# Optimization experiments

Measured on AMD Instinct MI355X. Metric: run time of the kernel, lower is better.

## Reference

```python
import jax, jax.numpy as jnp
import numpy as np

N = 100000
E = 1600000
IN_C, HID_C, OUT_C = 128, 128, 64


def setup_inputs() -> dict:
    key = jax.random.key(0)
    k_x, k_e, k_w1, k_w2 = jax.random.split(key, 4)
    x = jax.random.normal(k_x, (N, IN_C), dtype=jnp.float32)
    edge_index = jax.random.randint(k_e, (2, E), 0, N, dtype=jnp.int32)
    # nn.Linear default init: U(-1/sqrt(fan_in), 1/sqrt(fan_in)); bias init zeros per module
    lim1 = 1.0 / np.sqrt(IN_C)
    lim2 = 1.0 / np.sqrt(HID_C)
    W1 = jax.random.uniform(k_w1, (IN_C, HID_C), minval=-lim1, maxval=lim1, dtype=jnp.float32)
    b1 = jnp.zeros((HID_C,), dtype=jnp.float32)
    W2 = jax.random.uniform(k_w2, (HID_C, OUT_C), minval=-lim2, maxval=lim2, dtype=jnp.float32)
    b2 = jnp.zeros((OUT_C,), dtype=jnp.float32)
    return {"x": x, "edge_index": edge_index, "W1": W1, "b1": b1, "W2": W2, "b2": b2}


def _out_degree_gcn_conv(x, src, dst, W, b, n_nodes):
    # linear projection (no bias in lin)
    h = x @ W  # [N, out_c]
    # out-degree of each source node
    deg = jax.ops.segment_sum(jnp.ones((src.shape[0],), dtype=h.dtype), src, num_segments=n_nodes)
    deg_inv = 1.0 / jnp.maximum(deg, 1.0)  # clamp(min=1)
    h = h * deg_inv[:, None]
    # message: x_j = h[src]; aggregate: sum at dst
    out = jax.ops.segment_sum(h[src], dst, num_segments=n_nodes)  # [N, out_c]
    return out + b


def reference(x, edge_index, W1, b1, W2, b2):
    src, dst = edge_index[0], edge_index[1]
    n = x.shape[0]
    h = _out_degree_gcn_conv(x, src, dst, W1, b1, n)
    h = jax.nn.relu(h)
    # dropout p=0.0 -> identity
    out = _out_degree_gcn_conv(h, src, dst, W2, b2, n)
    return out
```

## Files before the change

kernel.cpp:

```cpp
#include <hip/hip_runtime.h>
#include <hip/hip_bf16.h>


typedef __attribute__((ext_vector_type(8))) short short8;
typedef __attribute__((ext_vector_type(4))) float floatx4;

__device__ inline unsigned short f2bf(float f) {
    union { float f; unsigned u; } v; v.f = f;
    return (unsigned short)((v.u + 0x8000u) >> 16);
}
__device__ inline float bf2f(unsigned b) {
    union { unsigned u; float f; } v; v.u = b << 16;
    return v.f;
}
__device__ inline float bf2f_hi(unsigned b) {
    union { unsigned u; float f; } v; v.u = b & 0xFFFF0000u;
    return v.f;
}

#define NBMAX 512
#define CAP   8192

__global__ __launch_bounds__(256) void convw_kernel(
    const float* __restrict__ W1, const float* __restrict__ W2,
    unsigned short* __restrict__ Wb1, unsigned short* __restrict__ Wb2,
    int* __restrict__ cnt)
{
    int i = blockIdx.x * 256 + threadIdx.x;
    if (i < NBMAX * 32) cnt[i] = 0;
    if (i < 128 * 128) {
        int k = i >> 7, n = i & 127;
        Wb1[n * 128 + k] = f2bf(W1[k * 128 + n]);
    }
    i -= 128 * 128;
    if (i >= 0 && i < 128 * 64) {
        int k = i >> 6, n = i & 63;
        Wb2[n * 128 + k] = f2bf(W2[k * 64 + n]);
    }
}

__global__ __launch_bounds__(256) void scatter2_kernel(
    const int* __restrict__ src, const int* __restrict__ dst, int E,
    int* __restrict__ cnt_d, int* __restrict__ cnt_s,
    unsigned* __restrict__ pairs, unsigned char* __restrict__ srcs_b, int NB,
    const float* __restrict__ x, unsigned short* __restrict__ xb, int NF8)
{
    const int EB = (E + 8191) / 8192;
    if ((int)blockIdx.x >= EB) {
        int i = ((int)blockIdx.x - EB) * 256 + threadIdx.x;
        if (i < NF8) {
            float4 a0 = ((const float4*)x)[(size_t)i * 2];
            float4 a1 = ((const float4*)x)[(size_t)i * 2 + 1];
            uint4 st;
            st.x = (unsigned)f2bf(a0.x) | ((unsigned)f2bf(a0.y) << 16);
            st.y = (unsigned)f2bf(a0.z) | ((unsigned)f2bf(a0.w) << 16);
            st.z = (unsigned)f2bf(a1.x) | ((unsigned)f2bf(a1.y) << 16);
            st.w = (unsigned)f2bf(a1.z) | ((unsigned)f2bf(a1.w) << 16);
            ((uint4*)xb)[i] = st;
        }
        return;
    }
    __shared__ int hd[NBMAX], bd[NBMAX], cd_[NBMAX];
    __shared__ int hs[NBMAX], bs[NBMAX], cs_[NBMAX];
    for (int i = threadIdx.x; i < NB; i += 256) { hd[i] = 0; cd_[i] = 0; hs[i] = 0; cs_[i] = 0; }
    __syncthreads();
    const int e0 = blockIdx.x * 8192;
    const int e1 = min(e0 + 8192, E);
    for (int i = e0 + threadIdx.x; i < e1; i += 256) {
        atomicAdd(&hd[dst[i] >> 8], 1);
        atomicAdd(&hs[src[i] >> 8], 1);
    }
    __syncthreads();
    for (int i = threadIdx.x; i < NB; i += 256) {
        if (hd[i]) bd[i] = atomicAdd(&cnt_d[i * 16], hd[i]);
        if (hs[i]) bs[i] = atomicAdd(&cnt_s[i * 16], hs[i]);
    }
    __syncthreads();
    for (int i = e0 + threadIdx.x; i < e1; i += 256) {
        int sv = src[i], dv = dst[i];
        int b = dv >> 8;
        int slot = atomicAdd(&cd_[b], 1);
        pairs[(size_t)b * CAP + bd[b] + slot] = ((unsigned)(dv & 255) << 24) | (unsigned)sv;
        int b2 = sv >> 8;
        int slot2 = atomicAdd(&cs_[b2], 1);
        srcs_b[(size_t)b2 * CAP + bs[b2] + slot2] = (unsigned char)(sv & 255);
    }
}

__global__ __launch_bounds__(256) void bucket_finalize_kernel(
    const unsigned* __restrict__ pairs, const unsigned char* __restrict__ srcs_b,
    const int* __restrict__ cnt_d, const int* __restrict__ cnt_s,
    int* __restrict__ sorted_src, int2* __restrict__ se,
    float* __restrict__ deg_inv, int N)
{
    const int b = blockIdx.x;
    const int node0 = b << 8;
    const int t = threadIdx.x;
    const size_t base = (size_t)b * CAP;
    __shared__ int hist[256];
    __shared__ int cur[256];
    __shared__ int pre[256];

    const int cd = cnt_d[b * 16];
    hist[t] = 0;
    __syncthreads();
    for (int i = t; i < cd; i += 256)
        atomicAdd(&hist[pairs[base + i] >> 24], 1);
    __syncthreads();
    int v = hist[t];
    int v4 = (v + 3) & ~3;
    pre[t] = v4;
    __syncthreads();
    for (int o = 1; o < 256; o <<= 1) {
        int add = (t >= o) ? pre[t - o] : 0;
        __syncthreads();
        pre[t] += add;
        __syncthreads();
    }
    int excl = pre[t] - v4;
    cur[t] = excl;
    if (node0 + t < N) {
        se[node0 + t] = make_int2((int)base + excl, (int)base + excl + v);
        for (int i = v; i < v4; ++i) sorted_src[base + excl + i] = N;
    }
    __syncthreads();
    for (int i = t; i < cd; i += 256) {
        unsigned p = pairs[base + i];
        int pos = atomicAdd(&cur[p >> 24], 1);
        sorted_src[base + pos] = (int)(p & 0xFFFFFFu);
    }

    __syncthreads();
    hist[t] = 0;
    __syncthreads();
    const int cs = cnt_s[b * 16];
    for (int i = t; i < cs; i += 256)
        atomicAdd(&hist[srcs_b[base + i]], 1);
    __syncthreads();
    if (node0 + t < N) {
        int d = hist[t];
        deg_inv[node0 + t] = 1.0f / (float)(d < 1 ? 1 : d);
    }
}

template <int NC, int SC>
__global__ __launch_bounds__(256) void gemm_mfma_kernel(
    const unsigned short* __restrict__ Ab, const unsigned short* __restrict__ Wb,
    const float* __restrict__ scale, unsigned short* __restrict__ Cb, int M)
{
    constexpr int NT = NC / 16;
    const int t = threadIdx.x;
    if (blockIdx.x == 0 && t < NC / 2)
        ((unsigned*)Cb)[(size_t)M * (NC / 2) + t] = 0;
    const int wm = t >> 6;
    const int lane = t & 63;
    const int lm = lane & 15;
    const int lk = (lane >> 4) * 8;

    const int r0 = blockIdx.x * 64 + wm * 16;
    int row = r0 + lm;
    if (row >= M) row = M - 1;

    floatx4 acc[NT];
#pragma unroll
    for (int j = 0; j < NT; ++j) acc[j] = (floatx4){0.f, 0.f, 0.f, 0.f};

#pragma unroll
    for (int kk = 0; kk < 4; ++kk) {
        const int kb = kk * 32 + lk;
        short8 af = *(const short8*)&Ab[(size_t)row * 128 + kb];
#pragma unroll
        for (int j = 0; j < NT; ++j) {
            short8 bfr = *(const short8*)&Wb[(size_t)(j * 16 + lm) * 128 + kb];
            acc[j] = __builtin_amdgcn_mfma_f32_16x16x32_bf16(af, bfr, acc[j], 0, 0, 0);
        }
    }

    const int rbase = r0 + (lane >> 4) * 4;
#pragma unroll
    for (int reg = 0; reg < 4; ++reg) {
        int rg = rbase + reg;
        if (rg < M) {
            float di = SC ? scale[rg] : 1.0f;
#pragma unroll
            for (int j = 0; j < NT; ++j)
                Cb[(size_t)rg * NC + j * 16 + lm] = f2bf(SC ? acc[j][reg] * di : acc[j][reg]);
        }
    }
}

#define LD128(vv, ii) uint2 vv = *(const uint2*)&val[(size_t)(ii) * 64 + 2 * l]
#define ACC8_128(I0, I1) do { \
    LD128(v0, I0.x); LD128(v1, I0.y); LD128(v2, I0.z); LD128(v3, I0.w); \
    LD128(v4, I1.x); LD128(v5, I1.y); LD128(v6, I1.z); LD128(v7, I1.w); \
    a0 += ((bf2f(v0.x & 0xFFFF) + bf2f(v1.x & 0xFFFF)) + (bf2f(v2.x & 0xFFFF) + bf2f(v3.x & 0xFFFF))) \
        + ((bf2f(v4.x & 0xFFFF) + bf2f(v5.x & 0xFFFF)) + (bf2f(v6.x & 0xFFFF) + bf2f(v7.x & 0xFFFF))); \
    a1 += ((bf2f_hi(v0.x) + bf2f_hi(v1.x)) + (bf2f_hi(v2.x) + bf2f_hi(v3.x))) \
        + ((bf2f_hi(v4.x) + bf2f_hi(v5.x)) + (bf2f_hi(v6.x) + bf2f_hi(v7.x))); \
    a2 += ((bf2f(v0.y & 0xFFFF) + bf2f(v1.y & 0xFFFF)) + (bf2f(v2.y & 0xFFFF) + bf2f(v3.y & 0xFFFF))) \
        + ((bf2f(v4.y & 0xFFFF) + bf2f(v5.y & 0xFFFF)) + (bf2f(v6.y & 0xFFFF) + bf2f(v7.y & 0xFFFF))); \
    a3 += ((bf2f_hi(v0.y) + bf2f_hi(v1.y)) + (bf2f_hi(v2.y) + bf2f_hi(v3.y))) \
        + ((bf2f_hi(v4.y) + bf2f_hi(v5.y)) + (bf2f_hi(v6.y) + bf2f_hi(v7.y))); \
} while (0)
#define ACC4_128(I0) do { \
    LD128(v0, I0.x); LD128(v1, I0.y); LD128(v2, I0.z); LD128(v3, I0.w); \
    a0 += (bf2f(v0.x & 0xFFFF) + bf2f(v1.x & 0xFFFF)) + (bf2f(v2.x & 0xFFFF) + bf2f(v3.x & 0xFFFF)); \
    a1 += (bf2f_hi(v0.x) + bf2f_hi(v1.x)) + (bf2f_hi(v2.x) + bf2f_hi(v3.x)); \
    a2 += (bf2f(v0.y & 0xFFFF) + bf2f(v1.y & 0xFFFF)) + (bf2f(v2.y & 0xFFFF) + bf2f(v3.y & 0xFFFF)); \
    a3 += (bf2f_hi(v0.y) + bf2f_hi(v1.y)) + (bf2f_hi(v2.y) + bf2f_hi(v3.y)); \
} while (0)

__global__ __launch_bounds__(256) void aggregate128_kernel(
    const int2* __restrict__ se, const int* __restrict__ sorted_src,
    const unsigned* __restrict__ val, const float* __restrict__ bias,
    const float* __restrict__ deg_inv, unsigned* __restrict__ outb, int N)
{
    const int hw = threadIdx.x >> 5;
    const int l = threadIdx.x & 31;
    for (int g = 0; g < 4; ++g) {
        int node = blockIdx.x * 32 + g * 8 + hw;
        if (node >= N) continue;
        int2 r = se[node];
        int e = r.x;
        const int end4 = r.x + ((r.y - r.x + 3) & ~3);
        float a0 = 0.f, a1 = 0.f, a2 = 0.f, a3 = 0.f;

        if (e + 8 <= end4) {
            int4 i0 = *(const int4*)&sorted_src[e];
            int4 i1 = *(const int4*)&sorted_src[e + 4];
            for (; e + 16 <= end4; e += 8) {
                int4 n0 = *(const int4*)&sorted_src[e + 8];
                int4 n1 = *(const int4*)&sorted_src[e + 12];
                ACC8_128(i0, i1);
                i0 = n0; i1 = n1;
            }
            ACC8_128(i0, i1);
            e += 8;
        }
        if (e < end4) {
            int4 i0 = *(const int4*)&sorted_src[e];
            ACC4_128(i0);
        }

        float di = deg_inv[node];
        float4 bv = *(const float4*)&bias[4 * l];
        a0 = fmaxf(a0 + bv.x, 0.f) * di;
        a1 = fmaxf(a1 + bv.y, 0.f) * di;
        a2 = fmaxf(a2 + bv.z, 0.f) * di;
        a3 = fmaxf(a3 + bv.w, 0.f) * di;
        uint2 o;
        o.x = (unsigned)f2bf(a0) | ((unsigned)f2bf(a1) << 16);
        o.y = (unsigned)f2bf(a2) | ((unsigned)f2bf(a3) << 16);
        *(uint2*)&outb[(size_t)node * 64 + 2 * l] = o;
    }
}

#define LD64(vv, ii) unsigned vv = val[(size_t)(ii) * 32 + l]
#define ACC8_64(I0, I1) do { \
    LD64(v0, I0.x); LD64(v1, I0.y); LD64(v2, I0.z); LD64(v3, I0.w); \
    LD64(v4, I1.x); LD64(v5, I1.y); LD64(v6, I1.z); LD64(v7, I1.w); \
    ax += ((bf2f(v0 & 0xFFFF) + bf2f(v1 & 0xFFFF)) + (bf2f(v2 & 0xFFFF) + bf2f(v3 & 0xFFFF))) \
        + ((bf2f(v4 & 0xFFFF) + bf2f(v5 & 0xFFFF)) + (bf2f(v6 & 0xFFFF) + bf2f(v7 & 0xFFFF))); \
    ay += ((bf2f_hi(v0) + bf2f_hi(v1)) + (bf2f_hi(v2) + bf2f_hi(v3))) \
        + ((bf2f_hi(v4) + bf2f_hi(v5)) + (bf2f_hi(v6) + bf2f_hi(v7))); \
} while (0)
#define ACC4_64(I0) do { \
    LD64(v0, I0.x); LD64(v1, I0.y); LD64(v2, I0.z); LD64(v3, I0.w); \
    ax += (bf2f(v0 & 0xFFFF) + bf2f(v1 & 0xFFFF)) + (bf2f(v2 & 0xFFFF) + bf2f(v3 & 0xFFFF)); \
    ay += (bf2f_hi(v0) + bf2f_hi(v1)) + (bf2f_hi(v2) + bf2f_hi(v3)); \
} while (0)

__global__ __launch_bounds__(256) void aggregate64_kernel(
    const int2* __restrict__ se, const int* __restrict__ sorted_src,
    const unsigned* __restrict__ val, const float* __restrict__ bias,
    float* __restrict__ out, int N)
{
    const int hw = threadIdx.x >> 5;
    const int l = threadIdx.x & 31;
    for (int g = 0; g < 4; ++g) {
        int node = blockIdx.x * 32 + g * 8 + hw;
        if (node >= N) continue;
        int2 r = se[node];
        int e = r.x;
        const int end4 = r.x + ((r.y - r.x + 3) & ~3);
        float ax = 0.f, ay = 0.f;

        if (e + 8 <= end4) {
            int4 i0 = *(const int4*)&sorted_src[e];
            int4 i1 = *(const int4*)&sorted_src[e + 4];
            for (; e + 16 <= end4; e += 8) {
                int4 n0 = *(const int4*)&sorted_src[e + 8];
                int4 n1 = *(const int4*)&sorted_src[e + 12];
                ACC8_64(i0, i1);
                i0 = n0; i1 = n1;
            }
            ACC8_64(i0, i1);
            e += 8;
        }
        if (e < end4) {
            int4 i0 = *(const int4*)&sorted_src[e];
            ACC4_64(i0);
        }

        float2 o = make_float2(ax + bias[2 * l], ay + bias[2 * l + 1]);
        *(float2*)&out[(size_t)node * 64 + 2 * l] = o;
    }
}

extern "C" void kernel_launch(void* const* d_in, const int* in_sizes, int n_in,
                              void* d_out, int out_size, void* d_ws, size_t ws_size,
                              hipStream_t stream) {
    const float* x  = (const float*)d_in[0];
    const int*   ei = (const int*)d_in[1];
    const float* W1 = (const float*)d_in[2];
    const float* b1 = (const float*)d_in[3];
    const float* W2 = (const float*)d_in[4];
    const float* b2 = (const float*)d_in[5];
    float* out = (float*)d_out;

    const int N = in_sizes[0] / 128;
    const int E = in_sizes[1] / 2;
    const int* src = ei;
    const int* dst = ei + E;
    const int NB = (N + 255) >> 8;

    char* ws = (char*)d_ws;
    size_t off = 0;
    auto alloc = [&](size_t bytes) {
        void* p = ws + off;
        off = (off + bytes + 255) & ~(size_t)255;
        return p;
    };
    float* deg_inv  = (float*)alloc((size_t)N * 4);
    int2*  se       = (int2*)alloc((size_t)N * 8);
    int*   cnt_d    = (int*)alloc((size_t)NBMAX * 16 * 4 * 2);
    int*   cnt_s    = cnt_d + (size_t)NBMAX * 16;
    unsigned short* Wb1 = (unsigned short*)alloc((size_t)128 * 128 * 2);
    unsigned short* Wb2 = (unsigned short*)alloc((size_t)64 * 128 * 2);
    unsigned*      pairs  = (unsigned*)alloc((size_t)NBMAX * CAP * 4);
    unsigned char* srcs_b = (unsigned char*)alloc((size_t)NBMAX * CAP);
    int*   sorted_src = (int*)alloc((size_t)NBMAX * CAP * 4);
    unsigned short* h    = (unsigned short*)alloc((size_t)(N + 1) * 128 * 2);
    unsigned short* out1 = (unsigned short*)alloc((size_t)N * 128 * 2);
    unsigned short* xb = out1;
    unsigned short* g = ((size_t)(N + 1) * 128 <= (size_t)NBMAX * CAP * 4)
                            ? (unsigned short*)pairs
                            : (unsigned short*)alloc((size_t)(N + 1) * 64 * 2);

    convw_kernel<<<96, 256, 0, stream>>>(W1, W2, Wb1, Wb2, cnt_d);

    const int EB = (E + 8191) / 8192;
    const int NF8 = (N * 128) / 8;
    const int CB = (NF8 + 255) / 256;
    scatter2_kernel<<<EB + CB, 256, 0, stream>>>(src, dst, E, cnt_d, cnt_s,
                                                 pairs, srcs_b, NB, x, xb, NF8);
    bucket_finalize_kernel<<<NB, 256, 0, stream>>>(pairs, srcs_b, cnt_d, cnt_s,
                                                   sorted_src, se, deg_inv, N);

    const int gblocks = (N + 63) / 64;
    const int ablocks = (N + 31) / 32;
    gemm_mfma_kernel<128, 1><<<gblocks, 256, 0, stream>>>(xb, Wb1, deg_inv, h, N);
    aggregate128_kernel<<<ablocks, 256, 0, stream>>>(se, sorted_src, (const unsigned*)h, b1,
                                                     deg_inv, (unsigned*)out1, N);
    gemm_mfma_kernel<64, 0><<<gblocks, 256, 0, stream>>>(out1, Wb2, nullptr, g, N);
    aggregate64_kernel<<<ablocks, 256, 0, stream>>>(se, sorted_src, (const unsigned*)g, b2, out, N);
}
```

Baseline: 316.8 us.

## Count out-degree with global atomics, enlarge scatter blocks, one node per half-warp

Replaces the per-bucket byte scatter of source ids plus the second histogram pass with direct global atomic increments into a per-node degree array, which is zeroed in the weight-conversion kernel. This removes the srcs_b buffer and its writes and reads. The scatter kernel moves to 1024-thread blocks. Both aggregate kernels now handle one node per half-warp with 8 nodes per block instead of looping over 32 nodes, giving four times more blocks. The trade is 1.6M global atomics on a 100K-entry array, which may contend.

```diff
diff --git a/kernel.cpp b/kernel.cpp
--- a/kernel.cpp
+++ b/kernel.cpp
@@ -24,10 +24,11 @@
 __global__ __launch_bounds__(256) void convw_kernel(
     const float* __restrict__ W1, const float* __restrict__ W2,
     unsigned short* __restrict__ Wb1, unsigned short* __restrict__ Wb2,
-    int* __restrict__ cnt)
+    int* __restrict__ cnt_d, int* __restrict__ deg_cnt, int N)
 {
     int i = blockIdx.x * 256 + threadIdx.x;
-    if (i < NBMAX * 32) cnt[i] = 0;
+    if (i < NBMAX * 16) cnt_d[i] = 0;
+    if (i < N) deg_cnt[i] = 0;
     if (i < 128 * 128) {
         int k = i >> 7, n = i & 127;
         Wb1[n * 128 + k] = f2bf(W1[k * 128 + n]);
@@ -39,15 +40,15 @@
     }
 }
 
-__global__ __launch_bounds__(256) void scatter2_kernel(
+__global__ __launch_bounds__(1024) void scatter2_kernel(
     const int* __restrict__ src, const int* __restrict__ dst, int E,
-    int* __restrict__ cnt_d, int* __restrict__ cnt_s,
-    unsigned* __restrict__ pairs, unsigned char* __restrict__ srcs_b, int NB,
+    int* __restrict__ cnt_d, int* __restrict__ deg_cnt,
+    unsigned* __restrict__ pairs, int NB,
     const float* __restrict__ x, unsigned short* __restrict__ xb, int NF8)
 {
     const int EB = (E + 8191) / 8192;
     if ((int)blockIdx.x >= EB) {
-        int i = ((int)blockIdx.x - EB) * 256 + threadIdx.x;
+        int i = ((int)blockIdx.x - EB) * 1024 + threadIdx.x;
         if (i < NF8) {
             float4 a0 = ((const float4*)x)[(size_t)i * 2];
             float4 a1 = ((const float4*)x)[(size_t)i * 2 + 1];
@@ -61,35 +62,30 @@
         return;
     }
     __shared__ int hd[NBMAX], bd[NBMAX], cd_[NBMAX];
-    __shared__ int hs[NBMAX], bs[NBMAX], cs_[NBMAX];
-    for (int i = threadIdx.x; i < NB; i += 256) { hd[i] = 0; cd_[i] = 0; hs[i] = 0; cs_[i] = 0; }
+    const int t = threadIdx.x;
+    for (int i = t; i < NB; i += 1024) { hd[i] = 0; cd_[i] = 0; }
     __syncthreads();
     const int e0 = blockIdx.x * 8192;
     const int e1 = min(e0 + 8192, E);
-    for (int i = e0 + threadIdx.x; i < e1; i += 256) {
+    for (int i = e0 + t; i < e1; i += 1024) {
         atomicAdd(&hd[dst[i] >> 8], 1);
-        atomicAdd(&hs[src[i] >> 8], 1);
-    }
-    __syncthreads();
-    for (int i = threadIdx.x; i < NB; i += 256) {
+        atomicAdd(&deg_cnt[src[i]], 1);
+    }
+    __syncthreads();
+    for (int i = t; i < NB; i += 1024)
         if (hd[i]) bd[i] = atomicAdd(&cnt_d[i * 16], hd[i]);
-        if (hs[i]) bs[i] = atomicAdd(&cnt_s[i * 16], hs[i]);
-    }
-    __syncthreads();
-    for (int i = e0 + threadIdx.x; i < e1; i += 256) {
+    __syncthreads();
+    for (int i = e0 + t; i < e1; i += 1024) {
         int sv = src[i], dv = dst[i];
         int b = dv >> 8;
         int slot = atomicAdd(&cd_[b], 1);
         pairs[(size_t)b * CAP + bd[b] + slot] = ((unsigned)(dv & 255) << 24) | (unsigned)sv;
-        int b2 = sv >> 8;
-        int slot2 = atomicAdd(&cs_[b2], 1);
-        srcs_b[(size_t)b2 * CAP + bs[b2] + slot2] = (unsigned char)(sv & 255);
     }
 }
 
 __global__ __launch_bounds__(256) void bucket_finalize_kernel(
-    const unsigned* __restrict__ pairs, const unsigned char* __restrict__ srcs_b,
-    const int* __restrict__ cnt_d, const int* __restrict__ cnt_s,
+    const unsigned* __restrict__ pairs, const int* __restrict__ cnt_d,
+    const int* __restrict__ deg_cnt,
     int* __restrict__ sorted_src, int2* __restrict__ se,
     float* __restrict__ deg_inv, int N)
 {
@@ -122,24 +118,14 @@
     if (node0 + t < N) {
         se[node0 + t] = make_int2((int)base + excl, (int)base + excl + v);
         for (int i = v; i < v4; ++i) sorted_src[base + excl + i] = N;
+        int d = deg_cnt[node0 + t];
+        deg_inv[node0 + t] = 1.0f / (float)(d < 1 ? 1 : d);
     }
     __syncthreads();
     for (int i = t; i < cd; i += 256) {
         unsigned p = pairs[base + i];
         int pos = atomicAdd(&cur[p >> 24], 1);
         sorted_src[base + pos] = (int)(p & 0xFFFFFFu);
-    }
-
-    __syncthreads();
-    hist[t] = 0;
-    __syncthreads();
-    const int cs = cnt_s[b * 16];
-    for (int i = t; i < cs; i += 256)
-        atomicAdd(&hist[srcs_b[base + i]], 1);
-    __syncthreads();
-    if (node0 + t < N) {
-        int d = hist[t];
-        deg_inv[node0 + t] = 1.0f / (float)(d < 1 ? 1 : d);
     }
 }
 
@@ -215,44 +201,41 @@
     const unsigned* __restrict__ val, const float* __restrict__ bias,
     const float* __restrict__ deg_inv, unsigned* __restrict__ outb, int N)
 {
-    const int hw = threadIdx.x >> 5;
-    const int l = threadIdx.x & 31;
-    for (int g = 0; g < 4; ++g) {
-        int node = blockIdx.x * 32 + g * 8 + hw;
-        if (node >= N) continue;
-        int2 r = se[node];
-        int e = r.x;
-        const int end4 = r.x + ((r.y - r.x + 3) & ~3);
-        float a0 = 0.f, a1 = 0.f, a2 = 0.f, a3 = 0.f;
-
-        if (e + 8 <= end4) {
-            int4 i0 = *(const int4*)&sorted_src[e];
-            int4 i1 = *(const int4*)&sorted_src[e + 4];
-            for (; e + 16 <= end4; e += 8) {
-                int4 n0 = *(const int4*)&sorted_src[e + 8];
-                int4 n1 = *(const int4*)&sorted_src[e + 12];
-                ACC8_128(i0, i1);
-                i0 = n0; i1 = n1;
-            }
+    int node = blockIdx.x * 8 + (threadIdx.x >> 5);
+    if (node >= N) return;
+    int l = threadIdx.x & 31;
+    int2 r = se[node];
+    int e = r.x;
+    const int end4 = r.x + ((r.y - r.x + 3) & ~3);
+    float a0 = 0.f, a1 = 0.f, a2 = 0.f, a3 = 0.f;
+
+    if (e + 8 <= end4) {
+        int4 i0 = *(const int4*)&sorted_src[e];
+        int4 i1 = *(const int4*)&sorted_src[e + 4];
+        for (; e + 16 <= end4; e += 8) {
+            int4 n0 = *(const int4*)&sorted_src[e + 8];
+            int4 n1 = *(const int4*)&sorted_src[e + 12];
             ACC8_128(i0, i1);
-            e += 8;
-        }
-        if (e < end4) {
-            int4 i0 = *(const int4*)&sorted_src[e];
-            ACC4_128(i0);
-        }
-
-        float di = deg_inv[node];
-        float4 bv = *(const float4*)&bias[4 * l];
-        a0 = fmaxf(a0 + bv.x, 0.f) * di;
-        a1 = fmaxf(a1 + bv.y, 0.f) * di;
-        a2 = fmaxf(a2 + bv.z, 0.f) * di;
-        a3 = fmaxf(a3 + bv.w, 0.f) * di;
-        uint2 o;
-        o.x = (unsigned)f2bf(a0) | ((unsigned)f2bf(a1) << 16);
-        o.y = (unsigned)f2bf(a2) | ((unsigned)f2bf(a3) << 16);
-        *(uint2*)&outb[(size_t)node * 64 + 2 * l] = o;
-    }
+            i0 = n0; i1 = n1;
+        }
+        ACC8_128(i0, i1);
+        e += 8;
+    }
+    if (e < end4) {
+        int4 i0 = *(const int4*)&sorted_src[e];
+        ACC4_128(i0);
+    }
+
+    float di = deg_inv[node];
+    float4 bv = *(const float4*)&bias[4 * l];
+    a0 = fmaxf(a0 + bv.x, 0.f) * di;
+    a1 = fmaxf(a1 + bv.y, 0.f) * di;
+    a2 = fmaxf(a2 + bv.z, 0.f) * di;
+    a3 = fmaxf(a3 + bv.w, 0.f) * di;
+    uint2 o;
+    o.x = (unsigned)f2bf(a0) | ((unsigned)f2bf(a1) << 16);
+    o.y = (unsigned)f2bf(a2) | ((unsigned)f2bf(a3) << 16);
+    *(uint2*)&outb[(size_t)node * 64 + 2 * l] = o;
 }
 
 #define LD64(vv, ii) unsigned vv = val[(size_t)(ii) * 32 + l]
@@ -275,36 +258,33 @@
     const unsigned* __restrict__ val, const float* __restrict__ bias,
     float* __restrict__ out, int N)
 {
-    const int hw = threadIdx.x >> 5;
-    const int l = threadIdx.x & 31;
-    for (int g = 0; g < 4; ++g) {
-        int node = blockIdx.x * 32 + g * 8 + hw;
-        if (node >= N) continue;
-        int2 r = se[node];
-        int e = r.x;
-        const int end4 = r.x + ((r.y - r.x + 3) & ~3);
-        float ax = 0.f, ay = 0.f;
-
-        if (e + 8 <= end4) {
-            int4 i0 = *(const int4*)&sorted_src[e];
-            int4 i1 = *(const int4*)&sorted_src[e + 4];
-            for (; e + 16 <= end4; e += 8) {
-                int4 n0 = *(const int4*)&sorted_src[e + 8];
-                int4 n1 = *(const int4*)&sorted_src[e + 12];
-                ACC8_64(i0, i1);
-                i0 = n0; i1 = n1;
-            }
+    int node = blockIdx.x * 8 + (threadIdx.x >> 5);
+    if (node >= N) return;
+    int l = threadIdx.x & 31;
+    int2 r = se[node];
+    int e = r.x;
+    const int end4 = r.x + ((r.y - r.x + 3) & ~3);
+    float ax = 0.f, ay = 0.f;
+
+    if (e + 8 <= end4) {
+        int4 i0 = *(const int4*)&sorted_src[e];
+        int4 i1 = *(const int4*)&sorted_src[e + 4];
+        for (; e + 16 <= end4; e += 8) {
+            int4 n0 = *(const int4*)&sorted_src[e + 8];
+            int4 n1 = *(const int4*)&sorted_src[e + 12];
             ACC8_64(i0, i1);
-            e += 8;
-        }
-        if (e < end4) {
-            int4 i0 = *(const int4*)&sorted_src[e];
-            ACC4_64(i0);
-        }
-
-        float2 o = make_float2(ax + bias[2 * l], ay + bias[2 * l + 1]);
-        *(float2*)&out[(size_t)node * 64 + 2 * l] = o;
-    }
+            i0 = n0; i1 = n1;
+        }
+        ACC8_64(i0, i1);
+        e += 8;
+    }
+    if (e < end4) {
+        int4 i0 = *(const int4*)&sorted_src[e];
+        ACC4_64(i0);
+    }
+
+    float2 o = make_float2(ax + bias[2 * l], ay + bias[2 * l + 1]);
+    *(float2*)&out[(size_t)node * 64 + 2 * l] = o;
 }
 
 extern "C" void kernel_launch(void* const* d_in, const int* in_sizes, int n_in,
@@ -332,13 +312,12 @@
         return p;
     };
     float* deg_inv  = (float*)alloc((size_t)N * 4);
+    int*   deg_cnt  = (int*)alloc((size_t)N * 4);
     int2*  se       = (int2*)alloc((size_t)N * 8);
-    int*   cnt_d    = (int*)alloc((size_t)NBMAX * 16 * 4 * 2);
-    int*   cnt_s    = cnt_d + (size_t)NBMAX * 16;
+    int*   cnt_d    = (int*)alloc((size_t)NBMAX * 16 * 4);
     unsigned short* Wb1 = (unsigned short*)alloc((size_t)128 * 128 * 2);
     unsigned short* Wb2 = (unsigned short*)alloc((size_t)64 * 128 * 2);
     unsigned*      pairs  = (unsigned*)alloc((size_t)NBMAX * CAP * 4);
-    unsigned char* srcs_b = (unsigned char*)alloc((size_t)NBMAX * CAP);
     int*   sorted_src = (int*)alloc((size_t)NBMAX * CAP * 4);
     unsigned short* h    = (unsigned short*)alloc((size_t)(N + 1) * 128 * 2);
     unsigned short* out1 = (unsigned short*)alloc((size_t)N * 128 * 2);
@@ -347,18 +326,19 @@
                             ? (unsigned short*)pairs
                             : (unsigned short*)alloc((size_t)(N + 1) * 64 * 2);
 
-    convw_kernel<<<96, 256, 0, stream>>>(W1, W2, Wb1, Wb2, cnt_d);
+    const int cwblocks = (N > 128 * 128 + 128 * 64 ? N + 255 : 128 * 128 + 128 * 64 + 255) / 256;
+    convw_kernel<<<cwblocks, 256, 0, stream>>>(W1, W2, Wb1, Wb2, cnt_d, deg_cnt, N);
 
     const int EB = (E + 8191) / 8192;
     const int NF8 = (N * 128) / 8;
-    const int CB = (NF8 + 255) / 256;
-    scatter2_kernel<<<EB + CB, 256, 0, stream>>>(src, dst, E, cnt_d, cnt_s,
-                                                 pairs, srcs_b, NB, x, xb, NF8);
-    bucket_finalize_kernel<<<NB, 256, 0, stream>>>(pairs, srcs_b, cnt_d, cnt_s,
+    const int CB = (NF8 + 1023) / 1024;
+    scatter2_kernel<<<EB + CB, 1024, 0, stream>>>(src, dst, E, cnt_d, deg_cnt,
+                                                  pairs, NB, x, xb, NF8);
+    bucket_finalize_kernel<<<NB, 256, 0, stream>>>(pairs, cnt_d, deg_cnt,
                                                    sorted_src, se, deg_inv, N);
 
     const int gblocks = (N + 63) / 64;
-    const int ablocks = (N + 31) / 32;
+    const int ablocks = (N + 7) / 8;
     gemm_mfma_kernel<128, 1><<<gblocks, 256, 0, stream>>>(xb, Wb1, deg_inv, h, N);
     aggregate128_kernel<<<ablocks, 256, 0, stream>>>(se, sorted_src, (const unsigned*)h, b1,
                                                      deg_inv, (unsigned*)out1, N);
```

New measurement: 327.5 us. 3.4% more time.

## Stage bucket scatter in shared memory for coalesced writes; one node per half-warp

Applied to the files above, without the earlier changes.

The edge bucketing kernel now sorts each chunk's entries by bucket in shared memory, using a local histogram and prefix scan, before writing them out. Each global write then lands in a contiguous run per bucket instead of a random address per edge. The kernel runs with 512 threads and handles the dst and src passes one after another, adding scans, a binary search per element and extra barriers. Separately, the aggregate kernels drop the 4-iteration node loop so each 32-lane group handles a single node, which launches more blocks and improves load balance.

```diff
diff --git a/kernel.cpp b/kernel.cpp
--- a/kernel.cpp
+++ b/kernel.cpp
@@ -20,6 +20,7 @@
 
 #define NBMAX 512
 #define CAP   8192
+#define CHUNK 8192
 
 __global__ __launch_bounds__(256) void convw_kernel(
     const float* __restrict__ W1, const float* __restrict__ W2,
@@ -39,15 +40,23 @@
     }
 }
 
-__global__ __launch_bounds__(256) void scatter2_kernel(
+#define SCAN512(lb, t)                                    \
+    for (int o = 1; o < 512; o <<= 1) {                   \
+        int add_ = ((t) >= o) ? lb[(t) - o] : 0;          \
+        __syncthreads();                                  \
+        lb[t] += add_;                                    \
+        __syncthreads();                                  \
+    }
+
+__global__ __launch_bounds__(512) void scatter2_kernel(
     const int* __restrict__ src, const int* __restrict__ dst, int E,
     int* __restrict__ cnt_d, int* __restrict__ cnt_s,
     unsigned* __restrict__ pairs, unsigned char* __restrict__ srcs_b, int NB,
     const float* __restrict__ x, unsigned short* __restrict__ xb, int NF8)
 {
-    const int EB = (E + 8191) / 8192;
+    const int EB = (E + CHUNK - 1) / CHUNK;
     if ((int)blockIdx.x >= EB) {
-        int i = ((int)blockIdx.x - EB) * 256 + threadIdx.x;
+        int i = ((int)blockIdx.x - EB) * 512 + threadIdx.x;
         if (i < NF8) {
             float4 a0 = ((const float4*)x)[(size_t)i * 2];
             float4 a1 = ((const float4*)x)[(size_t)i * 2 + 1];
@@ -60,30 +69,63 @@
         }
         return;
     }
-    __shared__ int hd[NBMAX], bd[NBMAX], cd_[NBMAX];
-    __shared__ int hs[NBMAX], bs[NBMAX], cs_[NBMAX];
-    for (int i = threadIdx.x; i < NB; i += 256) { hd[i] = 0; cd_[i] = 0; hs[i] = 0; cs_[i] = 0; }
-    __syncthreads();
-    const int e0 = blockIdx.x * 8192;
-    const int e1 = min(e0 + 8192, E);
-    for (int i = e0 + threadIdx.x; i < e1; i += 256) {
+    __shared__ int hd[NBMAX], lb[512], bd[NBMAX], cd_[NBMAX];
+    __shared__ unsigned staged[CHUNK];
+    const int t = threadIdx.x;
+    const int e0 = blockIdx.x * CHUNK;
+    const int e1 = min(e0 + CHUNK, E);
+    const int cnt = e1 - e0;
+
+    for (int i = t; i < NB; i += 512) { hd[i] = 0; cd_[i] = 0; }
+    __syncthreads();
+    for (int i = e0 + t; i < e1; i += 512)
         atomicAdd(&hd[dst[i] >> 8], 1);
-        atomicAdd(&hs[src[i] >> 8], 1);
-    }
-    __syncthreads();
-    for (int i = threadIdx.x; i < NB; i += 256) {
+    __syncthreads();
+    lb[t] = (t < NB) ? hd[t] : 0;
+    __syncthreads();
+    SCAN512(lb, t)
+    for (int i = t; i < NB; i += 512)
         if (hd[i]) bd[i] = atomicAdd(&cnt_d[i * 16], hd[i]);
-        if (hs[i]) bs[i] = atomicAdd(&cnt_s[i * 16], hs[i]);
-    }
-    __syncthreads();
-    for (int i = e0 + threadIdx.x; i < e1; i += 256) {
+    __syncthreads();
+    for (int i = e0 + t; i < e1; i += 512) {
         int sv = src[i], dv = dst[i];
         int b = dv >> 8;
         int slot = atomicAdd(&cd_[b], 1);
-        pairs[(size_t)b * CAP + bd[b] + slot] = ((unsigned)(dv & 255) << 24) | (unsigned)sv;
-        int b2 = sv >> 8;
-        int slot2 = atomicAdd(&cs_[b2], 1);
-        srcs_b[(size_t)b2 * CAP + bs[b2] + slot2] = (unsigned char)(sv & 255);
+        staged[lb[b] - hd[b] + slot] = ((unsigned)(dv & 255) << 24) | (unsigned)sv;
+    }
+    __syncthreads();
+    for (int i = t; i < cnt; i += 512) {
+        int lo = 0, hi = NB - 1;
+        while (lo < hi) { int mid = (lo + hi) >> 1; if (lb[mid] > i) hi = mid; else lo = mid + 1; }
+        int b = lo;
+        pairs[(size_t)b * CAP + bd[b] + (i - (lb[b] - hd[b]))] = staged[i];
+    }
+    __syncthreads();
+
+    unsigned char* stb = (unsigned char*)staged;
+    for (int i = t; i < NB; i += 512) { hd[i] = 0; cd_[i] = 0; }
+    __syncthreads();
+    for (int i = e0 + t; i < e1; i += 512)
+        atomicAdd(&hd[src[i] >> 8], 1);
+    __syncthreads();
+    lb[t] = (t < NB) ? hd[t] : 0;
+    __syncthreads();
+    SCAN512(lb, t)
+    for (int i = t; i < NB; i += 512)
+        if (hd[i]) bd[i] = atomicAdd(&cnt_s[i * 16], hd[i]);
+    __syncthreads();
+    for (int i = e0 + t; i < e1; i += 512) {
+        int sv = src[i];
+        int b = sv >> 8;
+        int slot = atomicAdd(&cd_[b], 1);
+        stb[lb[b] - hd[b] + slot] = (unsigned char)(sv & 255);
+    }
+    __syncthreads();
+    for (int i = t; i < cnt; i += 512) {
+        int lo = 0, hi = NB - 1;
+        while (lo < hi) { int mid = (lo + hi) >> 1; if (lb[mid] > i) hi = mid; else lo = mid + 1; }
+        int b = lo;
+        srcs_b[(size_t)b * CAP + bd[b] + (i - (lb[b] - hd[b]))] = stb[i];
     }
 }
 
@@ -215,44 +257,41 @@
     const unsigned* __restrict__ val, const float* __restrict__ bias,
     const float* __restrict__ deg_inv, unsigned* __restrict__ outb, int N)
 {
-    const int hw = threadIdx.x >> 5;
-    const int l = threadIdx.x & 31;
-    for (int g = 0; g < 4; ++g) {
-        int node = blockIdx.x * 32 + g * 8 + hw;
-        if (node >= N) continue;
-        int2 r = se[node];
-        int e = r.x;
-        const int end4 = r.x + ((r.y - r.x + 3) & ~3);
-        float a0 = 0.f, a1 = 0.f, a2 = 0.f, a3 = 0.f;
-
-        if (e + 8 <= end4) {
-            int4 i0 = *(const int4*)&sorted_src[e];
-            int4 i1 = *(const int4*)&sorted_src[e + 4];
-            for (; e + 16 <= end4; e += 8) {
-                int4 n0 = *(const int4*)&sorted_src[e + 8];
-                int4 n1 = *(const int4*)&sorted_src[e + 12];
-                ACC8_128(i0, i1);
-                i0 = n0; i1 = n1;
-            }
+    int node = blockIdx.x * 8 + (threadIdx.x >> 5);
+    if (node >= N) return;
+    int l = threadIdx.x & 31;
+    int2 r = se[node];
+    int e = r.x;
+    const int end4 = r.x + ((r.y - r.x + 3) & ~3);
+    float a0 = 0.f, a1 = 0.f, a2 = 0.f, a3 = 0.f;
+
+    if (e + 8 <= end4) {
+        int4 i0 = *(const int4*)&sorted_src[e];
+        int4 i1 = *(const int4*)&sorted_src[e + 4];
+        for (; e + 16 <= end4; e += 8) {
+            int4 n0 = *(const int4*)&sorted_src[e + 8];
+            int4 n1 = *(const int4*)&sorted_src[e + 12];
             ACC8_128(i0, i1);
-            e += 8;
+            i0 = n0; i1 = n1;
         }
-        if (e < end4) {
-            int4 i0 = *(const int4*)&sorted_src[e];
-            ACC4_128(i0);
-        }
-
-        float di = deg_inv[node];
-        float4 bv = *(const float4*)&bias[4 * l];
-        a0 = fmaxf(a0 + bv.x, 0.f) * di;
-        a1 = fmaxf(a1 + bv.y, 0.f) * di;
-        a2 = fmaxf(a2 + bv.z, 0.f) * di;
-        a3 = fmaxf(a3 + bv.w, 0.f) * di;
-        uint2 o;
-        o.x = (unsigned)f2bf(a0) | ((unsigned)f2bf(a1) << 16);
-        o.y = (unsigned)f2bf(a2) | ((unsigned)f2bf(a3) << 16);
-        *(uint2*)&outb[(size_t)node * 64 + 2 * l] = o;
-    }
+        ACC8_128(i0, i1);
+        e += 8;
+    }
+    if (e < end4) {
+        int4 i0 = *(const int4*)&sorted_src[e];
+        ACC4_128(i0);
+    }
+
+    float di = deg_inv[node];
+    float4 bv = *(const float4*)&bias[4 * l];
+    a0 = fmaxf(a0 + bv.x, 0.f) * di;
+    a1 = fmaxf(a1 + bv.y, 0.f) * di;
+    a2 = fmaxf(a2 + bv.z, 0.f) * di;
+    a3 = fmaxf(a3 + bv.w, 0.f) * di;
+    uint2 o;
+    o.x = (unsigned)f2bf(a0) | ((unsigned)f2bf(a1) << 16);
+    o.y = (unsigned)f2bf(a2) | ((unsigned)f2bf(a3) << 16);
+    *(uint2*)&outb[(size_t)node * 64 + 2 * l] = o;
 }
 
 #define LD64(vv, ii) unsigned vv = val[(size_t)(ii) * 32 + l]
@@ -275,36 +314,33 @@
     const unsigned* __restrict__ val, const float* __restrict__ bias,
     float* __restrict__ out, int N)
 {
-    const int hw = threadIdx.x >> 5;
-    const int l = threadIdx.x & 31;
-    for (int g = 0; g < 4; ++g) {
-        int node = blockIdx.x * 32 + g * 8 + hw;
-        if (node >= N) continue;
-        int2 r = se[node];
-        int e = r.x;
-        const int end4 = r.x + ((r.y - r.x + 3) & ~3);
-        float ax = 0.f, ay = 0.f;
-
-        if (e + 8 <= end4) {
-            int4 i0 = *(const int4*)&sorted_src[e];
-            int4 i1 = *(const int4*)&sorted_src[e + 4];
-            for (; e + 16 <= end4; e += 8) {
-                int4 n0 = *(const int4*)&sorted_src[e + 8];
-                int4 n1 = *(const int4*)&sorted_src[e + 12];
-                ACC8_64(i0, i1);
-                i0 = n0; i1 = n1;
-            }
+    int node = blockIdx.x * 8 + (threadIdx.x >> 5);
+    if (node >= N) return;
+    int l = threadIdx.x & 31;
+    int2 r = se[node];
+    int e = r.x;
+    const int end4 = r.x + ((r.y - r.x + 3) & ~3);
+    float ax = 0.f, ay = 0.f;
+
+    if (e + 8 <= end4) {
+        int4 i0 = *(const int4*)&sorted_src[e];
+        int4 i1 = *(const int4*)&sorted_src[e + 4];
+        for (; e + 16 <= end4; e += 8) {
+            int4 n0 = *(const int4*)&sorted_src[e + 8];
+            int4 n1 = *(const int4*)&sorted_src[e + 12];
             ACC8_64(i0, i1);
-            e += 8;
+            i0 = n0; i1 = n1;
         }
-        if (e < end4) {
-            int4 i0 = *(const int4*)&sorted_src[e];
-            ACC4_64(i0);
-        }
-
-        float2 o = make_float2(ax + bias[2 * l], ay + bias[2 * l + 1]);
-        *(float2*)&out[(size_t)node * 64 + 2 * l] = o;
-    }
+        ACC8_64(i0, i1);
+        e += 8;
+    }
+    if (e < end4) {
+        int4 i0 = *(const int4*)&sorted_src[e];
+        ACC4_64(i0);
+    }
+
+    float2 o = make_float2(ax + bias[2 * l], ay + bias[2 * l + 1]);
+    *(float2*)&out[(size_t)node * 64 + 2 * l] = o;
 }
 
 extern "C" void kernel_launch(void* const* d_in, const int* in_sizes, int n_in,
@@ -349,16 +385,16 @@
 
     convw_kernel<<<96, 256, 0, stream>>>(W1, W2, Wb1, Wb2, cnt_d);
 
-    const int EB = (E + 8191) / 8192;
+    const int EB = (E + CHUNK - 1) / CHUNK;
     const int NF8 = (N * 128) / 8;
-    const int CB = (NF8 + 255) / 256;
-    scatter2_kernel<<<EB + CB, 256, 0, stream>>>(src, dst, E, cnt_d, cnt_s,
+    const int CB = (NF8 + 511) / 512;
+    scatter2_kernel<<<EB + CB, 512, 0, stream>>>(src, dst, E, cnt_d, cnt_s,
                                                  pairs, srcs_b, NB, x, xb, NF8);
     bucket_finalize_kernel<<<NB, 256, 0, stream>>>(pairs, srcs_b, cnt_d, cnt_s,
                                                    sorted_src, se, deg_inv, N);
 
     const int gblocks = (N + 63) / 64;
-    const int ablocks = (N + 31) / 32;
+    const int ablocks = (N + 7) / 8;
     gemm_mfma_kernel<128, 1><<<gblocks, 256, 0, stream>>>(xb, Wb1, deg_inv, h, N);
     aggregate128_kernel<<<ablocks, 256, 0, stream>>>(se, sorted_src, (const unsigned*)h, b1,
                                                      deg_inv, (unsigned*)out1, N);
```

Measured after the change: 306.8 us. -3.1%, faster.
